# Performance work log

Hardware: AMD Instinct MI355X
Metric: run time of the kernel (lower is better)

## Reference

```python
import jax, jax.numpy as jnp
import numpy as np

D_MODEL = 1024
N_HEADS = 16
N_KV_HEADS = 4
HEAD_DIM = D_MODEL // N_HEADS
NUM_REP = N_HEADS // N_KV_HEADS
B, T = 2, 2048


def setup_inputs() -> dict:
    key = jax.random.key(0)
    ks = jax.random.split(key, 9)
    s = 0.02
    x = jax.random.normal(ks[0], (B, T, D_MODEL), dtype=jnp.float32)
    # causal mask: True = masked (matches torch masked_fill semantics)
    mask = jnp.triu(jnp.ones((T, T), dtype=bool), k=1)[None, None]
    kv_dim = N_KV_HEADS * HEAD_DIM
    return {
        "x": x,
        "mask": mask,
        "Wq": jax.random.normal(ks[1], (D_MODEL, D_MODEL), jnp.float32) * s,
        "bq": jnp.zeros((D_MODEL,), jnp.float32),
        "Wk": jax.random.normal(ks[2], (D_MODEL, kv_dim), jnp.float32) * s,
        "bk": jnp.zeros((kv_dim,), jnp.float32),
        "Wv": jax.random.normal(ks[3], (D_MODEL, kv_dim), jnp.float32) * s,
        "bv": jnp.zeros((kv_dim,), jnp.float32),
        "Wo": jax.random.normal(ks[4], (D_MODEL, D_MODEL), jnp.float32) * s,
        "bo": jnp.zeros((D_MODEL,), jnp.float32),
    }


def reference(x, mask, Wq, bq, Wk, bk, Wv, bv, Wo, bo):
    Bx, Tx, C = x.shape
    # projections
    q = (x @ Wq + bq).reshape(Bx, Tx, N_HEADS, HEAD_DIM).transpose(0, 2, 1, 3)  # (B,H,T,D)
    k = (x @ Wk + bk).reshape(Bx, Tx, N_KV_HEADS, HEAD_DIM)
    v = (x @ Wv + bv).reshape(Bx, Tx, N_KV_HEADS, HEAD_DIM)
    # repeat_kv: expand+reshape == repeat along head axis
    k = jnp.repeat(k, NUM_REP, axis=2).transpose(0, 2, 1, 3)  # (B,H,T,D)
    v = jnp.repeat(v, NUM_REP, axis=2).transpose(0, 2, 1, 3)
    scale = 1.0 / jnp.sqrt(jnp.asarray(HEAD_DIM, x.dtype))
    attn = jnp.einsum('bhtd,bhsd->bhts', q, k) * scale  # (B,H,T,T)
    attn = jnp.where(mask, -jnp.inf, attn)
    attn = jax.nn.softmax(attn, axis=-1)
    out = jnp.einsum('bhts,bhsd->bhtd', attn, v)
    out = out.transpose(0, 2, 1, 3).reshape(Bx, Tx, C)
    return out @ Wo + bo
```

## Files before the change

### kernel.cpp

```cpp
#include <hip/hip_runtime.h>
#include <hip/hip_bf16.h>
#include <cmath>
#include <stdint.h>


typedef __attribute__((ext_vector_type(4))) float f32x4;
typedef __attribute__((ext_vector_type(16))) float f32x16;
typedef __attribute__((ext_vector_type(8))) short s16x8;
typedef __attribute__((ext_vector_type(8))) unsigned short u16x8;

#define MFMA32(a, b, c) __builtin_amdgcn_mfma_f32_32x32x16_bf16(a, b, c, 0, 0, 0)

__device__ __forceinline__ unsigned short f2bf(float f) {
    unsigned int u = __float_as_uint(f);
    u += 0x7FFFu + ((u >> 16) & 1u);
    return (unsigned short)(u >> 16);
}

__device__ __forceinline__ unsigned int pktr(float lo, float hi) {
    return __builtin_amdgcn_perm(__float_as_uint(hi), __float_as_uint(lo), 0x07060302u);
}

__device__ __forceinline__ void async16(void* lds, const void* g) {
    __builtin_amdgcn_global_load_lds(
        (const __attribute__((address_space(1))) unsigned int*)g,
        (__attribute__((address_space(3))) unsigned int*)lds, 16, 0, 0);
}

__global__ __launch_bounds__(256) void prep(
        const float* __restrict__ x,
        const float* __restrict__ Wq, const float* __restrict__ Wk,
        const float* __restrict__ Wv, const float* __restrict__ Wo,
        const float* __restrict__ bq, const float* __restrict__ bk,
        const float* __restrict__ bv,
        unsigned short* __restrict__ xb, unsigned short* __restrict__ Wqkv,
        unsigned short* __restrict__ Wot, float* __restrict__ biasq, float qscale) {
    __shared__ unsigned short sx[128 * 72];
    __shared__ float tile[32][33];
    const int bid = blockIdx.x, tid = threadIdx.x;
    if (bid < 512) {
        const int mt = bid >> 4, kt = bid & 15;
#pragma unroll
        for (int i = 0; i < 8; ++i) {
            const int flat = (i * 256 + tid) * 4;
            const int row = flat >> 6, col = flat & 63;
            f32x4 ld = *reinterpret_cast<const f32x4*>(
                &x[(size_t)(mt * 128 + row) * 1024 + kt * 64 + col]);
            unsigned short* d = &sx[row * 72 + col];
            d[0] = f2bf(ld.x); d[1] = f2bf(ld.y); d[2] = f2bf(ld.z); d[3] = f2bf(ld.w);
        }
        __syncthreads();
#pragma unroll
        for (int j = 0; j < 4; ++j) {
            const int idx = j * 256 + tid;
            const int kb = idx >> 7, m = idx & 127;
            u16x8 v = *reinterpret_cast<const u16x8*>(&sx[m * 72 + kb * 8]);
            *reinterpret_cast<u16x8*>(
                &xb[(size_t)(((mt * 16 + kt) * 8 + kb) * 128 + m) * 8]) = v;
        }
    } else if (bid < 3072) {
        int id = bid - 512;
        const float* W; unsigned short* out; int N, nbase; float scale = 1.0f;
        if (id < 1024)      { W = Wq; out = Wqkv; N = 1024; nbase = 0;    scale = qscale; }
        else if (id < 1280) { W = Wk; out = Wqkv; N = 256;  nbase = 1024; id -= 1024; }
        else if (id < 1536) { W = Wv; out = Wqkv; N = 256;  nbase = 1280; id -= 1280; }
        else                { W = Wo; out = Wot;  N = 1024; nbase = 0;    id -= 1536; }
        const int nb = N >> 5;
        const int n0 = (id % nb) * 32, k0 = (id / nb) * 32;
        const int tx = tid & 31, ty = tid >> 5;
#pragma unroll
        for (int r = 0; r < 4; ++r)
            tile[ty + r * 8][tx] = W[(size_t)(k0 + ty + r * 8) * N + n0 + tx];
        __syncthreads();
        const int k = k0 + tx;
#pragma unroll
        for (int r = 0; r < 4; ++r) {
            const int n = nbase + n0 + ty + r * 8;
            size_t addr = (size_t)((n >> 6) * 16 + (k >> 6)) * 4096
                        + (size_t)((((k >> 3) & 7) * 64 + (n & 63)) * 8 + (k & 7));
            out[addr] = f2bf(tile[tx][ty + r * 8] * scale);
        }
    } else {
        const int i = (bid - 3072) * 256 + tid;
        if (i < 1024) biasq[i] = bq[i] * qscale;
        else if (i < 1280) biasq[i] = bk[i - 1024];
        else biasq[i] = bv[i - 1280];
    }
}

template <int EPI>
__global__ __launch_bounds__(256) void gemm_mn(
        const unsigned short* __restrict__ A, const unsigned short* __restrict__ Bt,
        const float* __restrict__ bias,
        unsigned short* __restrict__ oQ, unsigned short* __restrict__ oK,
        unsigned short* __restrict__ oV, float* __restrict__ oF) {
    __shared__ alignas(16) unsigned short sA[2][8 * 128 * 8];
    __shared__ alignas(16) unsigned short sB[2][8 * 64 * 8];
    const int tid = threadIdx.x;
    const int lane = tid & 63, w = tid >> 6;
    const int l31 = lane & 31, grp = lane >> 5;
    const int m0 = blockIdx.y * 128, n0 = blockIdx.x * 64;
    const int wm = w * 32;

    const unsigned short* Abase = A + (size_t)blockIdx.y * (16 * 8192) + (size_t)tid * 8;
    const unsigned short* Bbase = Bt + (size_t)blockIdx.x * (16 * 4096) + (size_t)tid * 8;

    f32x16 acc0 = {}, acc1 = {};

#pragma unroll
    for (int i = 0; i < 4; ++i)
        async16(&sA[0][(size_t)(i * 256 + (tid & 192)) * 8], Abase + (size_t)i * 2048);
#pragma unroll
    for (int i = 0; i < 2; ++i)
        async16(&sB[0][(size_t)(i * 256 + (tid & 192)) * 8], Bbase + (size_t)i * 2048);

    for (int kt = 0; kt < 16; ++kt) {
        const int cur = kt & 1;
        __syncthreads();
        if (kt < 15) {
            const unsigned short* ab = Abase + (size_t)(kt + 1) * 8192;
            const unsigned short* bb = Bbase + (size_t)(kt + 1) * 4096;
#pragma unroll
            for (int i = 0; i < 4; ++i)
                async16(&sA[cur ^ 1][(size_t)(i * 256 + (tid & 192)) * 8], ab + (size_t)i * 2048);
#pragma unroll
            for (int i = 0; i < 2; ++i)
                async16(&sB[cur ^ 1][(size_t)(i * 256 + (tid & 192)) * 8], bb + (size_t)i * 2048);
        }
#pragma unroll
        for (int kc = 0; kc < 4; ++kc) {
            const int kb = kc * 2 + grp;
            s16x8 a  = *reinterpret_cast<const s16x8*>(&sA[cur][(size_t)(kb * 128 + wm + l31) * 8]);
            s16x8 b0 = *reinterpret_cast<const s16x8*>(&sB[cur][(size_t)(kb * 64 + l31) * 8]);
            s16x8 b1 = *reinterpret_cast<const s16x8*>(&sB[cur][(size_t)(kb * 64 + 32 + l31) * 8]);
            acc0 = MFMA32(a, b0, acc0);
            acc1 = MFMA32(a, b1, acc1);
        }
    }
    const float bv0 = bias[n0 + l31], bv1 = bias[n0 + 32 + l31];
#pragma unroll
    for (int r = 0; r < 16; ++r) {
        const int row = m0 + wm + (r & 3) + 8 * (r >> 2) + 4 * grp;
        const float v0 = acc0[r] + bv0, v1 = acc1[r] + bv1;
        if (EPI == 0) {
            if (n0 < 1024) {
                oQ[(size_t)row * 1024 + n0 + l31] = f2bf(v0);
                oQ[(size_t)row * 1024 + n0 + 32 + l31] = f2bf(v1);
            } else if (n0 < 1280) {
                oK[(size_t)row * 256 + (n0 - 1024) + l31] = f2bf(v0);
                oK[(size_t)row * 256 + (n0 - 1024) + 32 + l31] = f2bf(v1);
            } else {
                oV[(size_t)(n0 - 1280 + l31) * 4096 + row] = f2bf(v0);
                oV[(size_t)(n0 - 1280 + 32 + l31) * 4096 + row] = f2bf(v1);
            }
        } else {
            oF[(size_t)row * 1024 + n0 + l31] = v0;
            oF[(size_t)row * 1024 + n0 + 32 + l31] = v1;
        }
    }
}

__global__ __launch_bounds__(512) void flash_attn(
        const unsigned short* __restrict__ Qb, const unsigned short* __restrict__ Kb,
        const unsigned short* __restrict__ Vt, unsigned short* __restrict__ Ot) {
    __shared__ alignas(16) unsigned short sK[2][64 * 72];
    __shared__ alignas(16) unsigned short sV[2][64 * 72];
    const int tid = threadIdx.x;
    const int lane = tid & 63, w = tid >> 6;
    const int ln = lane & 31, grp = lane >> 5;
    const int bh = blockIdx.x;
    const int qp = blockIdx.y;
    const int b = bh >> 4, h = bh & 15, kvh = h >> 2;
    const int myqt = (w < 4) ? qp : (15 - qp);
    const int nch_mine = 2 * myqt + 2;
    const int nch_all = 32 - 2 * qp;
    const int t0w = myqt * 128 + (w & 3) * 32;
    const int qrow_g = t0w + ln;

    const unsigned short* Qrow = Qb + (size_t)(b * 2048 + qrow_g) * 1024 + h * 64;
    s16x8 qf[4];
#pragma unroll
    for (int kk = 0; kk < 4; ++kk)
        qf[kk] = *reinterpret_cast<const s16x8*>(Qrow + kk * 16 + grp * 8);

    const unsigned short* Kbase = Kb + (size_t)(b * 2048) * 256 + kvh * 64;
    const unsigned short* Vbase = Vt + (size_t)(kvh * 64) * 4096 + (size_t)b * 2048;

    const int srow = tid >> 3, sd0 = (tid & 7) * 8;
    u16x8 kreg = *reinterpret_cast<const u16x8*>(Kbase + (size_t)srow * 256 + sd0);
    u16x8 vreg = *reinterpret_cast<const u16x8*>(Vbase + (size_t)srow * 4096 + sd0);

    f32x16 o0 = {}, o1 = {};
    float ltot = 0.f;

    for (int c = 0; c < nch_all; ++c) {
        unsigned short* bK = sK[c & 1];
        unsigned short* bV = sV[c & 1];
        *reinterpret_cast<u16x8*>(&bK[srow * 72 + sd0]) = kreg;
        *reinterpret_cast<u16x8*>(&bV[srow * 72 + sd0]) = vreg;
        __syncthreads();
        if (c + 1 < nch_all) {
            const int s1 = (c + 1) * 64;
            kreg = *reinterpret_cast<const u16x8*>(Kbase + (size_t)(s1 + srow) * 256 + sd0);
            vreg = *reinterpret_cast<const u16x8*>(Vbase + (size_t)srow * 4096 + s1 + sd0);
        }
        if (c < nch_mine) {
            const int s0 = c * 64;
            f32x16 st0 = {}, st1 = {};
#pragma unroll
            for (int kk = 0; kk < 4; ++kk) {
                s16x8 k0 = *reinterpret_cast<const s16x8*>(&bK[ln * 72 + kk * 16 + grp * 8]);
                s16x8 k1 = *reinterpret_cast<const s16x8*>(&bK[(32 + ln) * 72 + kk * 16 + grp * 8]);
                st0 = MFMA32(k0, qf[kk], st0);
                st1 = MFMA32(k1, qf[kk], st1);
            }
            if (s0 + 63 > t0w) {
#pragma unroll
                for (int r = 0; r < 16; ++r) {
                    const int keyo = s0 + (r & 3) + 8 * (r >> 2) + 4 * grp;
                    if (keyo > qrow_g)      st0[r] = -INFINITY;
                    if (keyo + 32 > qrow_g) st1[r] = -INFINITY;
                }
            }
            f32x16 p0, p1;
#pragma unroll
            for (int r = 0; r < 16; ++r) {
                p0[r] = __builtin_amdgcn_exp2f(st0[r]);
                p1[r] = __builtin_amdgcn_exp2f(st1[r]);
            }
            float a0 = 0.f, a1 = 0.f, a2 = 0.f, a3 = 0.f;
#pragma unroll
            for (int r = 0; r < 16; r += 2) {
                a0 += p0[r]; a1 += p0[r + 1];
                a2 += p1[r]; a3 += p1[r + 1];
            }
            ltot += (a0 + a1) + (a2 + a3);
#pragma unroll
            for (int kkp = 0; kkp < 4; ++kkp) {
                const f32x16& pm = (kkp < 2) ? p0 : p1;
                const int A4 = 8 * (kkp & 1);
                unsigned int pA0 = pktr(pm[A4 + 0], pm[A4 + 1]);
                unsigned int pA1 = pktr(pm[A4 + 2], pm[A4 + 3]);
                unsigned int pB0 = pktr(pm[A4 + 4], pm[A4 + 5]);
                unsigned int pB1 = pktr(pm[A4 + 6], pm[A4 + 7]);
                unsigned int x0 = (unsigned int)__shfl_xor((int)(grp ? pA0 : pB0), 32, 64);
                unsigned int x1 = (unsigned int)__shfl_xor((int)(grp ? pA1 : pB1), 32, 64);
                union { unsigned int u[4]; s16x8 v; } pf;
                pf.u[0] = grp ? x0 : pA0;
                pf.u[1] = grp ? x1 : pA1;
                pf.u[2] = grp ? pB0 : x0;
                pf.u[3] = grp ? pB1 : x1;
                s16x8 v0 = *reinterpret_cast<const s16x8*>(&bV[ln * 72 + kkp * 16 + grp * 8]);
                s16x8 v1 = *reinterpret_cast<const s16x8*>(&bV[(32 + ln) * 72 + kkp * 16 + grp * 8]);
                o0 = MFMA32(pf.v, v0, o0);
                o1 = MFMA32(pf.v, v1, o1);
            }
        }
    }

    const float lfull = ltot + __shfl_xor(ltot, 32, 64);
    const float rl = 1.0f / lfull;
    unsigned short* Otb = Ot + (size_t)((b * 16 + myqt) * 16 + h) * 8192
                             + (size_t)(ln >> 3) * 1024 + (ln & 7);
#pragma unroll
    for (int r = 0; r < 16; ++r) {
        const int row = (r & 3) + 8 * (r >> 2) + 4 * grp;
        const float rr = __shfl(rl, row, 64);
        const size_t off = (size_t)((w & 3) * 32 + row) * 8;
        Otb[off]        = f2bf(o0[r] * rr);
        Otb[off + 4096] = f2bf(o1[r] * rr);
    }
}

extern "C" void kernel_launch(void* const* d_in, const int* in_sizes, int n_in,
                              void* d_out, int out_size, void* d_ws, size_t ws_size,
                              hipStream_t stream) {
    const float* x  = (const float*)d_in[0];
    const float* Wq = (const float*)d_in[2];
    const float* bq = (const float*)d_in[3];
    const float* Wk = (const float*)d_in[4];
    const float* bk = (const float*)d_in[5];
    const float* Wv = (const float*)d_in[6];
    const float* bv = (const float*)d_in[7];
    const float* Wo = (const float*)d_in[8];
    const float* bo = (const float*)d_in[9];
    float* out = (float*)d_out;

    char* ws = (char*)d_ws;
    unsigned short* xb    = (unsigned short*)(ws);
    unsigned short* Wqkv  = (unsigned short*)(ws + (8u  << 20));
    unsigned short* Wot   = (unsigned short*)(ws + (12u << 20));
    float*          biasq = (float*)         (ws + (15u << 20));
    unsigned short* Qb    = (unsigned short*)(ws + (16u << 20));
    unsigned short* Kb    = (unsigned short*)(ws + (24u << 20));
    unsigned short* Vtp   = (unsigned short*)(ws + (26u << 20));
    unsigned short* Otl   = (unsigned short*)(ws + (28u << 20));

    const float qscale = 0.125f * 1.4426950408889634f;

    prep<<<3078, 256, 0, stream>>>(x, Wq, Wk, Wv, Wo, bq, bk, bv,
                                   xb, Wqkv, Wot, biasq, qscale);
    gemm_mn<0><<<dim3(24, 32), 256, 0, stream>>>(xb, Wqkv, biasq, Qb, Kb, Vtp, nullptr);
    flash_attn<<<dim3(32, 8), 512, 0, stream>>>(Qb, Kb, Vtp, Otl);
    gemm_mn<1><<<dim3(16, 32), 256, 0, stream>>>(Otl, Wot, bo, nullptr, nullptr, nullptr, out);
}
```

Baseline: 174.2 us.

## Software-pipeline PV MFMAs in attention and stage V-projection stores through LDS

The flash attention loop now holds each chunk's packed P fragments and V operands in registers and issues the P·V MFMAs one iteration later, after the next chunk's loads, so they overlap with the next QK^T and softmax. Warps whose last chunk is not followed by another loop iteration flush the pending MFMAs after the loop. Separately, the QKV GEMM epilogue for the transposed V output is staged through a merged shared-memory buffer, so it writes 16-byte coalesced rows instead of scattered 2-byte transposed stores. The costs are more live registers per thread in a 512-thread attention block, which may limit occupancy or cause spills, and extra barriers in the V epilogue.

```diff
diff --git a/kernel.cpp b/kernel.cpp
--- a/kernel.cpp
+++ b/kernel.cpp
@@ -94,8 +94,7 @@
         const float* __restrict__ bias,
         unsigned short* __restrict__ oQ, unsigned short* __restrict__ oK,
         unsigned short* __restrict__ oV, float* __restrict__ oF) {
-    __shared__ alignas(16) unsigned short sA[2][8 * 128 * 8];
-    __shared__ alignas(16) unsigned short sB[2][8 * 64 * 8];
+    __shared__ alignas(16) unsigned short smem[24576];
     const int tid = threadIdx.x;
     const int lane = tid & 63, w = tid >> 6;
     const int l31 = lane & 31, grp = lane >> 5;
@@ -109,35 +108,57 @@
 
 #pragma unroll
     for (int i = 0; i < 4; ++i)
-        async16(&sA[0][(size_t)(i * 256 + (tid & 192)) * 8], Abase + (size_t)i * 2048);
+        async16(&smem[(size_t)(i * 256 + (tid & 192)) * 8], Abase + (size_t)i * 2048);
 #pragma unroll
     for (int i = 0; i < 2; ++i)
-        async16(&sB[0][(size_t)(i * 256 + (tid & 192)) * 8], Bbase + (size_t)i * 2048);
+        async16(&smem[16384 + (size_t)(i * 256 + (tid & 192)) * 8], Bbase + (size_t)i * 2048);
 
     for (int kt = 0; kt < 16; ++kt) {
         const int cur = kt & 1;
+        unsigned short* cA = smem + cur * 8192;
+        unsigned short* cB = smem + 16384 + cur * 4096;
         __syncthreads();
         if (kt < 15) {
+            unsigned short* nA = smem + (cur ^ 1) * 8192;
+            unsigned short* nB = smem + 16384 + (cur ^ 1) * 4096;
             const unsigned short* ab = Abase + (size_t)(kt + 1) * 8192;
             const unsigned short* bb = Bbase + (size_t)(kt + 1) * 4096;
 #pragma unroll
             for (int i = 0; i < 4; ++i)
-                async16(&sA[cur ^ 1][(size_t)(i * 256 + (tid & 192)) * 8], ab + (size_t)i * 2048);
+                async16(&nA[(size_t)(i * 256 + (tid & 192)) * 8], ab + (size_t)i * 2048);
 #pragma unroll
             for (int i = 0; i < 2; ++i)
-                async16(&sB[cur ^ 1][(size_t)(i * 256 + (tid & 192)) * 8], bb + (size_t)i * 2048);
+                async16(&nB[(size_t)(i * 256 + (tid & 192)) * 8], bb + (size_t)i * 2048);
         }
 #pragma unroll
         for (int kc = 0; kc < 4; ++kc) {
             const int kb = kc * 2 + grp;
-            s16x8 a  = *reinterpret_cast<const s16x8*>(&sA[cur][(size_t)(kb * 128 + wm + l31) * 8]);
-            s16x8 b0 = *reinterpret_cast<const s16x8*>(&sB[cur][(size_t)(kb * 64 + l31) * 8]);
-            s16x8 b1 = *reinterpret_cast<const s16x8*>(&sB[cur][(size_t)(kb * 64 + 32 + l31) * 8]);
+            s16x8 a  = *reinterpret_cast<const s16x8*>(&cA[(size_t)(kb * 128 + wm + l31) * 8]);
+            s16x8 b0 = *reinterpret_cast<const s16x8*>(&cB[(size_t)(kb * 64 + l31) * 8]);
+            s16x8 b1 = *reinterpret_cast<const s16x8*>(&cB[(size_t)(kb * 64 + 32 + l31) * 8]);
             acc0 = MFMA32(a, b0, acc0);
             acc1 = MFMA32(a, b1, acc1);
         }
     }
     const float bv0 = bias[n0 + l31], bv1 = bias[n0 + 32 + l31];
+    if (EPI == 0 && n0 >= 1280) {
+        __syncthreads();
+#pragma unroll
+        for (int r = 0; r < 16; ++r) {
+            const int m = wm + (r & 3) + 8 * (r >> 2) + 4 * grp;
+            smem[(size_t)l31 * 136 + m] = f2bf(acc0[r] + bv0);
+            smem[(size_t)(l31 + 32) * 136 + m] = f2bf(acc1[r] + bv1);
+        }
+        __syncthreads();
+#pragma unroll
+        for (int i = 0; i < 4; ++i) {
+            const int id = i * 256 + tid;
+            const int n = id >> 4, mc = id & 15;
+            u16x8 v = *reinterpret_cast<const u16x8*>(&smem[(size_t)n * 136 + mc * 8]);
+            *reinterpret_cast<u16x8*>(&oV[(size_t)(n0 - 1280 + n) * 4096 + m0 + mc * 8]) = v;
+        }
+        return;
+    }
 #pragma unroll
     for (int r = 0; r < 16; ++r) {
         const int row = m0 + wm + (r & 3) + 8 * (r >> 2) + 4 * grp;
@@ -146,12 +167,9 @@
             if (n0 < 1024) {
                 oQ[(size_t)row * 1024 + n0 + l31] = f2bf(v0);
                 oQ[(size_t)row * 1024 + n0 + 32 + l31] = f2bf(v1);
-            } else if (n0 < 1280) {
+            } else {
                 oK[(size_t)row * 256 + (n0 - 1024) + l31] = f2bf(v0);
                 oK[(size_t)row * 256 + (n0 - 1024) + 32 + l31] = f2bf(v1);
-            } else {
-                oV[(size_t)(n0 - 1280 + l31) * 4096 + row] = f2bf(v0);
-                oV[(size_t)(n0 - 1280 + 32 + l31) * 4096 + row] = f2bf(v1);
             }
         } else {
             oF[(size_t)row * 1024 + n0 + l31] = v0;
@@ -192,6 +210,8 @@
 
     f32x16 o0 = {}, o1 = {};
     float ltot = 0.f;
+    s16x8 pfv[4];
+    s16x8 vp0[4], vp1[4];
 
     for (int c = 0; c < nch_all; ++c) {
         unsigned short* bK = sK[c & 1];
@@ -204,8 +224,20 @@
             kreg = *reinterpret_cast<const u16x8*>(Kbase + (size_t)(s1 + srow) * 256 + sd0);
             vreg = *reinterpret_cast<const u16x8*>(Vbase + (size_t)srow * 4096 + s1 + sd0);
         }
+        if (c >= 1 && c <= nch_mine) {
+#pragma unroll
+            for (int kkp = 0; kkp < 4; ++kkp) {
+                o0 = MFMA32(pfv[kkp], vp0[kkp], o0);
+                o1 = MFMA32(pfv[kkp], vp1[kkp], o1);
+            }
+        }
         if (c < nch_mine) {
             const int s0 = c * 64;
+#pragma unroll
+            for (int kkp = 0; kkp < 4; ++kkp) {
+                vp0[kkp] = *reinterpret_cast<const s16x8*>(&bV[ln * 72 + kkp * 16 + grp * 8]);
+                vp1[kkp] = *reinterpret_cast<const s16x8*>(&bV[(32 + ln) * 72 + kkp * 16 + grp * 8]);
+            }
             f32x16 st0 = {}, st1 = {};
 #pragma unroll
             for (int kk = 0; kk < 4; ++kk) {
@@ -250,11 +282,15 @@
                 pf.u[1] = grp ? x1 : pA1;
                 pf.u[2] = grp ? pB0 : x0;
                 pf.u[3] = grp ? pB1 : x1;
-                s16x8 v0 = *reinterpret_cast<const s16x8*>(&bV[ln * 72 + kkp * 16 + grp * 8]);
-                s16x8 v1 = *reinterpret_cast<const s16x8*>(&bV[(32 + ln) * 72 + kkp * 16 + grp * 8]);
-                o0 = MFMA32(pf.v, v0, o0);
-                o1 = MFMA32(pf.v, v1, o1);
-            }
+                pfv[kkp] = pf.v;
+            }
+        }
+    }
+    if (w >= 4) {
+#pragma unroll
+        for (int kkp = 0; kkp < 4; ++kkp) {
+            o0 = MFMA32(pfv[kkp], vp0[kkp], o0);
+            o1 = MFMA32(pfv[kkp], vp1[kkp], o1);
         }
     }
 
```

Result: faster. 168.7 us (-3.1%).
